# Kernel tuning notes

Hardware: AMD Instinct MI355X
Metric: run time of the kernel (lower is better)

Reference implementation:

```python
import jax, jax.numpy as jnp
from jax import lax
import numpy as np

B, CIN, CP, H, W = 16, 64, 64, 64, 64
K1 = 3   # deformable kernel
K2 = 5   # parallel conv kernel
EPS = 1e-5


def conv2d(x, w, stride, pad):
    return lax.conv_general_dilated(
        x, w, (stride, stride), [(pad, pad), (pad, pad)],
        dimension_numbers=('NCHW', 'OIHW', 'NCHW'))


def batchnorm(x, g, b, m, v):
    scale = g / jnp.sqrt(v + EPS)
    return (x - m[None, :, None, None]) * scale[None, :, None, None] + b[None, :, None, None]


def deform_conv2d(x, offset, weight, stride, pad):
    # x: [B,Cin,H,W], offset: [B,2*K*K,Ho,Wo] (dy,dx interleaved per kernel tap, torchvision layout)
    Bn, Cin, Hn, Wn = x.shape
    Cout, _, K, _ = weight.shape
    KK = K * K
    Ho, Wo = offset.shape[2], offset.shape[3]
    off = offset.reshape(Bn, KK, 2, Ho, Wo)
    dy, dx = off[:, :, 0], off[:, :, 1]                      # [B,KK,Ho,Wo]
    ky, kx = jnp.meshgrid(jnp.arange(K), jnp.arange(K), indexing='ij')
    ky = ky.reshape(KK).astype(x.dtype)
    kx = kx.reshape(KK).astype(x.dtype)
    base_y = (jnp.arange(Ho) * stride - pad).astype(x.dtype)
    base_x = (jnp.arange(Wo) * stride - pad).astype(x.dtype)
    ys = base_y[None, None, :, None] + ky[None, :, None, None] + dy  # [B,KK,Ho,Wo]
    xs = base_x[None, None, None, :] + kx[None, :, None, None] + dx
    y0 = jnp.floor(ys); x0 = jnp.floor(xs)
    wy1 = ys - y0; wx1 = xs - x0
    wy0 = 1.0 - wy1; wx0 = 1.0 - wx1
    flat = x.reshape(Bn, Cin, Hn * Wn)

    def gather(yi, xi):
        valid = ((yi >= 0) & (yi <= Hn - 1) & (xi >= 0) & (xi <= Wn - 1))
        yc = jnp.clip(yi, 0, Hn - 1).astype(jnp.int32)
        xc = jnp.clip(xi, 0, Wn - 1).astype(jnp.int32)
        idx = (yc * Wn + xc).reshape(Bn, -1)                 # [B,KK*Ho*Wo]
        g = jax.vmap(lambda f, i: jnp.take(f, i, axis=1))(flat, idx)
        g = g.reshape(Bn, Cin, KK, Ho, Wo)
        return g * valid.astype(x.dtype)[:, None]

    val = (gather(y0, x0) * (wy0 * wx0)[:, None]
           + gather(y0, x0 + 1) * (wy0 * wx1)[:, None]
           + gather(y0 + 1, x0) * (wy1 * wx0)[:, None]
           + gather(y0 + 1, x0 + 1) * (wy1 * wx1)[:, None])   # [B,Cin,KK,Ho,Wo]
    w_r = weight.reshape(Cout, Cin, KK)
    return jnp.einsum('bcknm,ock->bonm', val, w_r)


def setup_inputs():
    key = jax.random.key(0)
    ks = jax.random.split(key, 18)
    f32 = jnp.float32
    x = jax.random.normal(ks[0], (B, CIN, H, W), f32)
    w_off = jax.random.normal(ks[1], (2 * K1 * K1, CIN, 3, 3), f32) * 0.01
    b_off = jnp.zeros((2 * K1 * K1,), f32)
    w1 = jax.random.normal(ks[2], (CP, CIN, K1, K1), f32) / np.sqrt(CIN * K1 * K1)
    w3 = jax.random.normal(ks[3], (CP, CIN, K2, K2), f32) / np.sqrt(CIN * K2 * K2)
    w2 = jax.random.normal(ks[4], (CP, CP, 3, 3), f32) / np.sqrt(CP * 9)
    def bn(i):
        g = jax.random.uniform(ks[5 + 4 * i], (CP,), f32, 0.5, 1.5)
        b = jax.random.normal(ks[6 + 4 * i], (CP,), f32) * 0.1
        m = jax.random.normal(ks[7 + 4 * i], (CP,), f32) * 0.1
        v = jax.random.uniform(ks[8 + 4 * i], (CP,), f32, 0.5, 1.5)
        return g, b, m, v
    g1, b1, m1, v1 = bn(0)
    g3, b3, m3, v3 = bn(1)
    g2, b2, m2, v2 = bn(2)
    return dict(x=x, w_off=w_off, b_off=b_off, w1=w1, g1=g1, b1=b1, m1=m1, v1=v1,
                w3=w3, g3=g3, b3=b3, m3=m3, v3=v3, w2=w2, g2=g2, b2=b2, m2=m2, v2=v2)


def reference(x, w_off, b_off, w1, g1, b1, m1, v1, w3, g3, b3, m3, v3, w2, g2, b2, m2, v2):
    offset1 = conv2d(x, w_off, 1, 1) + b_off[None, :, None, None]
    out = jax.nn.relu(batchnorm(deform_conv2d(x, offset1, w1, 1, 1), g1, b1, m1, v1))
    out_1 = jax.nn.relu(batchnorm(conv2d(x, w3, 1, 2), g3, b3, m3, v3))
    out = out + out_1
    out = batchnorm(conv2d(out, w2, 1, 1), g2, b2, m2, v2)
    out = out + x  # identity shortcut (stride=1, in_planes==planes)
    return jax.nn.relu(out)
```

## Files before the change

kernel.cpp:

```cpp
#include <hip/hip_runtime.h>
#include <hip/hip_bf16.h>


#define HWv 4096
#define EPSv 1e-5f

typedef __attribute__((ext_vector_type(8))) short bf16x8;
typedef __attribute__((ext_vector_type(16))) float f32x16;
typedef __attribute__((ext_vector_type(2))) float f32x2;

__device__ inline ushort f2bf(float f) {
  __hip_bfloat16 h = __float2bfloat16(f);
  return *(ushort*)&h;
}
__device__ inline float bf2f(ushort u) {
  unsigned int t = ((unsigned int)u) << 16;
  union { unsigned int i; float f; } c; c.i = t; return c.f;
}
__device__ inline float bitsf(unsigned int u) {
  union { unsigned int i; float f; } c; c.i = u; return c.f;
}

__global__ __launch_bounds__(256) void prep_kernel(
    const float* __restrict__ x, const float* __restrict__ w3,
    const float* __restrict__ w2, const float* __restrict__ w1,
    const float* __restrict__ w_off,
    ushort* __restrict__ xT, ushort* __restrict__ w3F,
    ushort* __restrict__ w2F, ushort* __restrict__ w1F,
    ushort* __restrict__ wofF) {
  __shared__ float tile[64][65];
  const int blk = blockIdx.x;
  if (blk < 1024) {
    const int y = blk & 63, b = blk >> 6;
    for (int i = threadIdx.x; i < 4096; i += 256) {
      int ci = i >> 6, xx = i & 63;
      tile[ci][xx] = x[(((size_t)b * 64 + ci) * 64 + y) * 64 + xx];
    }
    __syncthreads();
    for (int i = threadIdx.x; i < 2048; i += 256) {
      int xx = i >> 5, cip = (i & 31) * 2;
      ushort2 v;
      v.x = f2bf(tile[cip][xx]);
      v.y = f2bf(tile[cip + 1][xx]);
      *(ushort2*)&xT[(((size_t)b * 64 + y) * 64 + xx) * 64 + cip] = v;
    }
    return;
  }
  int idx = (blk - 1024) * 256 + threadIdx.x;
  if (idx < 102400) {
    int j = idx & 7, lane = (idx >> 3) & 63, ks = (idx >> 9) & 3;
    int half = (idx >> 11) & 1, kk = idx >> 12;
    int ln = lane & 31, kh = lane >> 5;
    int co = half * 32 + ln, ci = ks * 16 + kh * 8 + j;
    w3F[idx] = f2bf(w3[(co * 64 + ci) * 25 + kk]);
    return;
  }
  idx -= 102400;
  if (idx < 36864) {
    int j = idx & 7, lane = (idx >> 3) & 63, ks = (idx >> 9) & 3;
    int half = (idx >> 11) & 1, kk = idx >> 12;
    int ln = lane & 31, kh = lane >> 5;
    int co = half * 32 + ln, ci = ks * 16 + kh * 8 + j;
    w2F[idx] = f2bf(w2[(co * 64 + ci) * 9 + kk]);
    return;
  }
  idx -= 36864;
  if (idx < 36864) {
    int j = idx & 7, lane = (idx >> 3) & 63, ks = (idx >> 9) & 3;
    int half = (idx >> 11) & 1, kk = idx >> 12;
    int ln = lane & 31, kh = lane >> 5;
    int co = half * 32 + ln, ci = ks * 16 + kh * 8 + j;
    w1F[idx] = f2bf(w1[(co * 64 + ci) * 9 + kk]);
    return;
  }
  idx -= 36864;
  if (idx < 18432) {
    int j = idx & 7, lane = (idx >> 3) & 63, ks = (idx >> 9) & 3;
    int kk = idx >> 11;
    int ln = lane & 31, kh = lane >> 5;
    int ci = ks * 16 + kh * 8 + j;
    wofF[idx] = f2bf(ln < 18 ? w_off[(ln * 64 + ci) * 9 + kk] : 0.f);
  }
}

__device__ __forceinline__ bf16x8 blend4(bf16x8 va, bf16x8 vb, bf16x8 vc, bf16x8 vd,
                                         f32x2 w00v, f32x2 w01v, f32x2 w10v, f32x2 w11v) {
  const unsigned int* ua = (const unsigned int*)&va;
  const unsigned int* ub = (const unsigned int*)&vb;
  const unsigned int* uc = (const unsigned int*)&vc;
  const unsigned int* ud = (const unsigned int*)&vd;
  bf16x8 f;
  ushort2* fo = (ushort2*)&f;
#pragma unroll
  for (int d = 0; d < 4; ++d) {
    f32x2 av = {bitsf(ua[d] << 16), bitsf(ua[d] & 0xFFFF0000u)};
    f32x2 bv = {bitsf(ub[d] << 16), bitsf(ub[d] & 0xFFFF0000u)};
    f32x2 cv = {bitsf(uc[d] << 16), bitsf(uc[d] & 0xFFFF0000u)};
    f32x2 dv = {bitsf(ud[d] << 16), bitsf(ud[d] & 0xFFFF0000u)};
    f32x2 r = w00v * av + w01v * bv + w10v * cv + w11v * dv;
    __hip_bfloat162 h2 = __float22bfloat162_rn(make_float2(r.x, r.y));
    fo[d] = *(ushort2*)&h2;
  }
  return f;
}

__global__ __launch_bounds__(256, 2) void fused_kernel(
    const ushort* __restrict__ xT, const ushort* __restrict__ wofF,
    const float* __restrict__ b_off, const ushort* __restrict__ w1F,
    const ushort* __restrict__ w3F,
    const float* __restrict__ g1, const float* __restrict__ b1,
    const float* __restrict__ m1, const float* __restrict__ v1,
    const float* __restrict__ g3, const float* __restrict__ b3,
    const float* __restrict__ m3, const float* __restrict__ v3,
    ushort* __restrict__ s1T) {
  __shared__ __align__(16) uint4 ldsx[6 * 68 * 8];
  __shared__ float stash[2 * 64 * 18];
  __shared__ float bn1s[64], bn1b[64], bn3s[64], bn3b[64];

  const int tid = threadIdx.x;
  const int wv = tid >> 6, lane = tid & 63;
  const int ln = lane & 31, kh = lane >> 5;
  const int r = wv >> 1, nt = wv & 1;
  const int y0 = blockIdx.x * 2, b = blockIdx.y;
  const int y = y0 + r, px = nt * 32 + ln;
  const uint4* xT4 = (const uint4*)xT;
  const bool interior = (y0 >= 2 && y0 <= 60);

  if (tid < 64) {
    float s = g1[tid] * rsqrtf(v1[tid] + EPSv);
    bn1s[tid] = s; bn1b[tid] = b1[tid] - m1[tid] * s;
    float s3 = g3[tid] * rsqrtf(v3[tid] + EPSv);
    bn3s[tid] = s3; bn3b[tid] = b3[tid] - m3[tid] * s3;
  }
  for (int i = tid; i < 6 * 68 * 8; i += 256) {
    int tr = i / (68 * 8), rem = i % (68 * 8);
    int col = rem >> 3, c = rem & 7;
    int ysrc = min(max(y0 - 2 + tr, 0), 63);
    int xcol = col - 2;
    uint4 v = make_uint4(0, 0, 0, 0);
    if (xcol >= 0 && xcol <= 63)
      v = xT4[((size_t)((b * 64 + ysrc) * 64 + xcol)) * 8 + c];
    ldsx[(tr * 68 + col) * 8 + (c ^ (col & 7))] = v;
  }
  __syncthreads();

  f32x16 acco;
#pragma unroll
  for (int j = 0; j < 16; ++j) acco[j] = 0.f;
  if (interior) {
#pragma unroll
    for (int kk = 0; kk < 9; ++kk) {
      const int ky = kk / 3, kx = kk % 3;
      const int tr = r + ky + 1;
      const int col = px + kx + 1;
      bf16x8 af[4], bf[4];
#pragma unroll
      for (int ks = 0; ks < 4; ++ks)
        af[ks] = *(const bf16x8*)&wofF[(size_t)((kk * 4 + ks) * 64 + lane) * 8];
#pragma unroll
      for (int ks = 0; ks < 4; ++ks) {
        int c = ks * 2 + kh;
        bf[ks] = *(const bf16x8*)&ldsx[(tr * 68 + col) * 8 + (c ^ (col & 7))];
      }
#pragma unroll
      for (int ks = 0; ks < 4; ++ks)
        acco = __builtin_amdgcn_mfma_f32_32x32x16_bf16(af[ks], bf[ks], acco, 0, 0, 0);
    }
  } else {
#pragma unroll
    for (int kk = 0; kk < 9; ++kk) {
      const int ky = kk / 3, kx = kk % 3;
      const int yy = y - 1 + ky;
      if (yy >= 0 && yy <= 63) {
        const int tr = yy - (y0 - 2);
        const int col = px + kx + 1;
#pragma unroll
        for (int ks = 0; ks < 4; ++ks) {
          int c = ks * 2 + kh;
          bf16x8 af = *(const bf16x8*)&wofF[(size_t)((kk * 4 + ks) * 64 + lane) * 8];
          bf16x8 bf = *(const bf16x8*)&ldsx[(tr * 68 + col) * 8 + (c ^ (col & 7))];
          acco = __builtin_amdgcn_mfma_f32_32x32x16_bf16(af, bf, acco, 0, 0, 0);
        }
      }
    }
  }
#pragma unroll
  for (int reg = 0; reg < 16; ++reg) {
    int co = (reg & 3) + 8 * (reg >> 2) + 4 * kh;
    if (co < 18)
      stash[(r * 64 + px) * 18 + co] = acco[reg] + b_off[co];
  }
  __syncthreads();

  float dyv[9], dxv[9];
#pragma unroll
  for (int kk = 0; kk < 9; ++kk) {
    dyv[kk] = stash[(r * 64 + px) * 18 + 2 * kk];
    dxv[kk] = stash[(r * 64 + px) * 18 + 2 * kk + 1];
  }
  bool fast = true;
#pragma unroll
  for (int kk = 0; kk < 9; ++kk) {
    int iy0 = (int)floorf((float)(y - 1 + kk / 3) + dyv[kk]);
    int iy1 = iy0 + 1;
    bool ok0 = (iy0 < 0) || (iy0 > 63) || (iy0 >= y0 - 2 && iy0 <= y0 + 3);
    bool ok1 = (iy1 < 0) || (iy1 > 63) || (iy1 >= y0 - 2 && iy1 <= y0 + 3);
    fast = fast && ok0 && ok1;
  }

  f32x16 accd0, accd1;
#pragma unroll
  for (int j = 0; j < 16; ++j) { accd0[j] = 0.f; accd1[j] = 0.f; }
  const ushort* xb = xT + (size_t)b * 64 * 64 * 64;

  if (__ballot(!fast) == 0ull) {
#pragma unroll
    for (int kk = 0; kk < 9; ++kk) {
      const int ky = kk / 3, kx = kk % 3;
      float ys = (float)(y - 1 + ky) + dyv[kk];
      float xs = (float)(px - 1 + kx) + dxv[kk];
      float y0f = floorf(ys), x0f = floorf(xs);
      float wy1 = ys - y0f, wx1 = xs - x0f;
      float wy0 = 1.f - wy1, wx0 = 1.f - wx1;
      int iy0 = (int)y0f, ix0 = (int)x0f;
      int iy1 = iy0 + 1, ix1 = ix0 + 1;
      float vy0 = (iy0 >= 0 && iy0 <= 63) ? 1.f : 0.f;
      float vy1 = (iy1 >= 0 && iy1 <= 63) ? 1.f : 0.f;
      float vx0 = (ix0 >= 0 && ix0 <= 63) ? 1.f : 0.f;
      float vx1 = (ix1 >= 0 && ix1 <= 63) ? 1.f : 0.f;
      int x0c = min(max(ix0, 0), 63), x1c = min(max(ix1, 0), 63);
      float w00 = wy0 * wx0 * vy0 * vx0;
      float w01 = wy0 * wx1 * vy0 * vx1;
      float w10 = wy1 * wx0 * vy1 * vx0;
      float w11 = wy1 * wx1 * vy1 * vx1;
      int tr0 = min(max(iy0 - (y0 - 2), 0), 5);
      int tr1 = min(max(iy1 - (y0 - 2), 0), 5);
      int c0 = x0c + 2, c1 = x1c + 2;
      f32x2 w00v = {w00, w00}, w01v = {w01, w01};
      f32x2 w10v = {w10, w10}, w11v = {w11, w11};

      bf16x8 a0[4], a1[4], va[4], vb[4], vc[4], vd[4];
#pragma unroll
      for (int ks = 0; ks < 4; ++ks) {
        a0[ks] = *(const bf16x8*)&w1F[(size_t)(((kk * 2 + 0) * 4 + ks) * 64 + lane) * 8];
        a1[ks] = *(const bf16x8*)&w1F[(size_t)(((kk * 2 + 1) * 4 + ks) * 64 + lane) * 8];
      }
#pragma unroll
      for (int ks = 0; ks < 4; ++ks) {
        int c = ks * 2 + kh;
        va[ks] = *(const bf16x8*)&ldsx[(tr0 * 68 + c0) * 8 + (c ^ (c0 & 7))];
        vb[ks] = *(const bf16x8*)&ldsx[(tr0 * 68 + c1) * 8 + (c ^ (c1 & 7))];
        vc[ks] = *(const bf16x8*)&ldsx[(tr1 * 68 + c0) * 8 + (c ^ (c0 & 7))];
        vd[ks] = *(const bf16x8*)&ldsx[(tr1 * 68 + c1) * 8 + (c ^ (c1 & 7))];
      }
#pragma unroll
      for (int ks = 0; ks < 4; ++ks) {
        bf16x8 f = blend4(va[ks], vb[ks], vc[ks], vd[ks], w00v, w01v, w10v, w11v);
        accd0 = __builtin_amdgcn_mfma_f32_32x32x16_bf16(a0[ks], f, accd0, 0, 0, 0);
        accd1 = __builtin_amdgcn_mfma_f32_32x32x16_bf16(a1[ks], f, accd1, 0, 0, 0);
      }
    }
  } else {
#pragma unroll
    for (int kk = 0; kk < 9; ++kk) {
      const int ky = kk / 3, kx = kk % 3;
      float ys = (float)(y - 1 + ky) + dyv[kk];
      float xs = (float)(px - 1 + kx) + dxv[kk];
      float y0f = floorf(ys), x0f = floorf(xs);
      float wy1 = ys - y0f, wx1 = xs - x0f;
      float wy0 = 1.f - wy1, wx0 = 1.f - wx1;
      int iy0 = (int)y0f, ix0 = (int)x0f;
      int iy1 = iy0 + 1, ix1 = ix0 + 1;
      float vy0 = (iy0 >= 0 && iy0 <= 63) ? 1.f : 0.f;
      float vy1 = (iy1 >= 0 && iy1 <= 63) ? 1.f : 0.f;
      float vx0 = (ix0 >= 0 && ix0 <= 63) ? 1.f : 0.f;
      float vx1 = (ix1 >= 0 && ix1 <= 63) ? 1.f : 0.f;
      int x0c = min(max(ix0, 0), 63), x1c = min(max(ix1, 0), 63);
      float w00 = wy0 * wx0 * vy0 * vx0;
      float w01 = wy0 * wx1 * vy0 * vx1;
      float w10 = wy1 * wx0 * vy1 * vx0;
      float w11 = wy1 * wx1 * vy1 * vx1;
      int tr0 = min(max(iy0 - (y0 - 2), 0), 5);
      int tr1 = min(max(iy1 - (y0 - 2), 0), 5);
      int c0 = x0c + 2, c1 = x1c + 2;
      f32x2 w00v = {w00, w00}, w01v = {w01, w01};
      f32x2 w10v = {w10, w10}, w11v = {w11, w11};

      bf16x8 frag[4];
#pragma unroll
      for (int ks = 0; ks < 4; ++ks) {
        int c = ks * 2 + kh;
        bf16x8 va = *(const bf16x8*)&ldsx[(tr0 * 68 + c0) * 8 + (c ^ (c0 & 7))];
        bf16x8 vb = *(const bf16x8*)&ldsx[(tr0 * 68 + c1) * 8 + (c ^ (c1 & 7))];
        bf16x8 vc = *(const bf16x8*)&ldsx[(tr1 * 68 + c0) * 8 + (c ^ (c0 & 7))];
        bf16x8 vd = *(const bf16x8*)&ldsx[(tr1 * 68 + c1) * 8 + (c ^ (c1 & 7))];
        frag[ks] = blend4(va, vb, vc, vd, w00v, w01v, w10v, w11v);
      }
      if (!fast) {
        int y0c = min(max(iy0, 0), 63), y1c = min(max(iy1, 0), 63);
        const ushort* p00 = xb + (y0c * 64 + x0c) * 64 + kh * 8;
        const ushort* p01 = xb + (y0c * 64 + x1c) * 64 + kh * 8;
        const ushort* p10 = xb + (y1c * 64 + x0c) * 64 + kh * 8;
        const ushort* p11 = xb + (y1c * 64 + x1c) * 64 + kh * 8;
#pragma unroll
        for (int ks = 0; ks < 4; ++ks) {
          bf16x8 va = *(const bf16x8*)(p00 + ks * 16);
          bf16x8 vb = *(const bf16x8*)(p01 + ks * 16);
          bf16x8 vc = *(const bf16x8*)(p10 + ks * 16);
          bf16x8 vd = *(const bf16x8*)(p11 + ks * 16);
          frag[ks] = blend4(va, vb, vc, vd, w00v, w01v, w10v, w11v);
        }
      }
#pragma unroll
      for (int ks = 0; ks < 4; ++ks) {
        bf16x8 a0 = *(const bf16x8*)&w1F[(size_t)(((kk * 2 + 0) * 4 + ks) * 64 + lane) * 8];
        bf16x8 a1 = *(const bf16x8*)&w1F[(size_t)(((kk * 2 + 1) * 4 + ks) * 64 + lane) * 8];
        accd0 = __builtin_amdgcn_mfma_f32_32x32x16_bf16(a0, frag[ks], accd0, 0, 0, 0);
        accd1 = __builtin_amdgcn_mfma_f32_32x32x16_bf16(a1, frag[ks], accd1, 0, 0, 0);
      }
    }
  }

  f32x16 acc50, acc51;
#pragma unroll
  for (int j = 0; j < 16; ++j) { acc50[j] = 0.f; acc51[j] = 0.f; }
  if (interior) {
#pragma unroll
    for (int kk = 0; kk < 25; ++kk) {
      const int ky = kk / 5, kx = kk % 5;
      const int tr = r + ky;
      const int col = px + kx;
      bf16x8 a0[4], a1[4], bfv[4];
#pragma unroll
      for (int ks = 0; ks < 4; ++ks) {
        a0[ks] = *(const bf16x8*)&w3F[(size_t)(((kk * 2 + 0) * 4 + ks) * 64 + lane) * 8];
        a1[ks] = *(const bf16x8*)&w3F[(size_t)(((kk * 2 + 1) * 4 + ks) * 64 + lane) * 8];
      }
#pragma unroll
      for (int ks = 0; ks < 4; ++ks) {
        int c = ks * 2 + kh;
        bfv[ks] = *(const bf16x8*)&ldsx[(tr * 68 + col) * 8 + (c ^ (col & 7))];
      }
#pragma unroll
      for (int ks = 0; ks < 4; ++ks) {
        acc50 = __builtin_amdgcn_mfma_f32_32x32x16_bf16(a0[ks], bfv[ks], acc50, 0, 0, 0);
        acc51 = __builtin_amdgcn_mfma_f32_32x32x16_bf16(a1[ks], bfv[ks], acc51, 0, 0, 0);
      }
    }
  } else {
#pragma unroll
    for (int kk = 0; kk < 25; ++kk) {
      const int ky = kk / 5, kx = kk % 5;
      const int yy = y - 2 + ky;
      if (yy >= 0 && yy <= 63) {
        const int tr = r + ky;
        const int col = px + kx;
#pragma unroll
        for (int ks = 0; ks < 4; ++ks) {
          int c = ks * 2 + kh;
          bf16x8 bf = *(const bf16x8*)&ldsx[(tr * 68 + col) * 8 + (c ^ (col & 7))];
          bf16x8 a0 = *(const bf16x8*)&w3F[(size_t)(((kk * 2 + 0) * 4 + ks) * 64 + lane) * 8];
          bf16x8 a1 = *(const bf16x8*)&w3F[(size_t)(((kk * 2 + 1) * 4 + ks) * 64 + lane) * 8];
          acc50 = __builtin_amdgcn_mfma_f32_32x32x16_bf16(a0, bf, acc50, 0, 0, 0);
          acc51 = __builtin_amdgcn_mfma_f32_32x32x16_bf16(a1, bf, acc51, 0, 0, 0);
        }
      }
    }
  }

  ushort* op = s1T + ((size_t)((b * 64 + y) * 64 + px)) * 64;
#pragma unroll
  for (int q = 0; q < 4; ++q) {
    int co0 = 8 * q + 4 * kh;
    float vv[4];
#pragma unroll
    for (int rr = 0; rr < 4; ++rr) {
      int co = co0 + rr;
      float vd = accd0[q * 4 + rr] * bn1s[co] + bn1b[co];
      vd = vd > 0.f ? vd : 0.f;
      float v5 = acc50[q * 4 + rr] * bn3s[co] + bn3b[co];
      v5 = v5 > 0.f ? v5 : 0.f;
      vv[rr] = vd + v5;
    }
    ushort4 st;
    st.x = f2bf(vv[0]); st.y = f2bf(vv[1]); st.z = f2bf(vv[2]); st.w = f2bf(vv[3]);
    *(ushort4*)(op + co0) = st;
#pragma unroll
    for (int rr = 0; rr < 4; ++rr) {
      int co = co0 + 32 + rr;
      float vd = accd1[q * 4 + rr] * bn1s[co] + bn1b[co];
      vd = vd > 0.f ? vd : 0.f;
      float v5 = acc51[q * 4 + rr] * bn3s[co] + bn3b[co];
      v5 = v5 > 0.f ? v5 : 0.f;
      vv[rr] = vd + v5;
    }
    st.x = f2bf(vv[0]); st.y = f2bf(vv[1]); st.z = f2bf(vv[2]); st.w = f2bf(vv[3]);
    *(ushort4*)(op + co0 + 32) = st;
  }
}

__global__ __launch_bounds__(256, 2) void conv3_mfma_kernel(
    const ushort* __restrict__ s1T, const ushort* __restrict__ w2F,
    const float* __restrict__ g2, const float* __restrict__ b2,
    const float* __restrict__ m2, const float* __restrict__ v2,
    const float* __restrict__ x, float* __restrict__ out) {
  __shared__ __align__(16) uint4 Bt[3 * 66 * 8];
  __shared__ float sc[64], bi[64];
  const int tid = threadIdx.x;
  if (tid < 64) {
    float s = g2[tid] * rsqrtf(v2[tid] + EPSv);
    sc[tid] = s;
    bi[tid] = b2[tid] - m2[tid] * s;
  }
  const int y = blockIdx.x, b = blockIdx.y;
  const int wv = tid >> 6, lane = tid & 63;
  const int ln = lane & 31, kh = lane >> 5;
  const int mh = wv & 1, nt = wv >> 1;
  const int px = nt * 32 + ln;
  const uint4* s1T4 = (const uint4*)s1T;

  for (int i = tid; i < 3 * 66 * 8; i += 256) {
    int tr = i / (66 * 8), rem = i % (66 * 8);
    int col = rem >> 3, c = rem & 7;
    int yy = y - 1 + tr, xcol = col - 1;
    uint4 v = make_uint4(0, 0, 0, 0);
    if (yy >= 0 && yy <= 63 && xcol >= 0 && xcol <= 63)
      v = s1T4[((size_t)((b * 64 + yy) * 64 + xcol)) * 8 + c];
    Bt[(tr * 66 + col) * 8 + (c ^ (col & 7))] = v;
  }
  __syncthreads();

  f32x16 acc;
#pragma unroll
  for (int j = 0; j < 16; ++j) acc[j] = 0.f;

#pragma unroll
  for (int kk = 0; kk < 9; ++kk) {
    const int ky = kk / 3, kx = kk % 3;
    const int col = px + kx;
    bf16x8 af[4], bfr[4];
#pragma unroll
    for (int ccb = 0; ccb < 4; ++ccb)
      af[ccb] = *(const bf16x8*)&w2F[(size_t)(((kk * 2 + mh) * 4 + ccb) * 64 + lane) * 8];
#pragma unroll
    for (int ccb = 0; ccb < 4; ++ccb) {
      int c = ccb * 2 + kh;
      bfr[ccb] = *(const bf16x8*)&Bt[(ky * 66 + col) * 8 + (c ^ (col & 7))];
    }
#pragma unroll
    for (int ccb = 0; ccb < 4; ++ccb)
      acc = __builtin_amdgcn_mfma_f32_32x32x16_bf16(af[ccb], bfr[ccb], acc, 0, 0, 0);
  }
#pragma unroll
  for (int reg = 0; reg < 16; ++reg) {
    int co = (reg & 3) + 8 * (reg >> 2) + 4 * kh + mh * 32;
    size_t o = (((size_t)b * 64 + co) * 64 + y) * 64 + px;
    float v = acc[reg] * sc[co] + bi[co] + x[o];
    out[o] = v > 0.f ? v : 0.f;
  }
}

extern "C" void kernel_launch(void* const* d_in, const int* in_sizes, int n_in,
                              void* d_out, int out_size, void* d_ws, size_t ws_size,
                              hipStream_t stream) {
  const float* x     = (const float*)d_in[0];
  const float* w_off = (const float*)d_in[1];
  const float* b_off = (const float*)d_in[2];
  const float* w1    = (const float*)d_in[3];
  const float* g1    = (const float*)d_in[4];
  const float* b1    = (const float*)d_in[5];
  const float* m1    = (const float*)d_in[6];
  const float* v1    = (const float*)d_in[7];
  const float* w3    = (const float*)d_in[8];
  const float* g3    = (const float*)d_in[9];
  const float* b3    = (const float*)d_in[10];
  const float* m3    = (const float*)d_in[11];
  const float* v3    = (const float*)d_in[12];
  const float* w2    = (const float*)d_in[13];
  const float* g2    = (const float*)d_in[14];
  const float* b2    = (const float*)d_in[15];
  const float* m2    = (const float*)d_in[16];
  const float* v2    = (const float*)d_in[17];
  float* out = (float*)d_out;

  ushort* xT   = (ushort*)d_ws;
  ushort* s1T  = xT + (size_t)16 * 64 * HWv;
  ushort* w3F  = s1T + (size_t)16 * 64 * HWv;
  ushort* w2F  = w3F + 102400;
  ushort* w1F  = w2F + 36864;
  ushort* wofF = w1F + 36864;

  prep_kernel<<<dim3(1024 + 760), dim3(256), 0, stream>>>(x, w3, w2, w1, w_off,
                                                          xT, w3F, w2F, w1F, wofF);
  fused_kernel<<<dim3(32, 16), dim3(256), 0, stream>>>(xT, wofF, b_off, w1F, w3F,
                                                       g1, b1, m1, v1, g3, b3, m3, v3,
                                                       s1T);
  conv3_mfma_kernel<<<dim3(64, 16), dim3(256), 0, stream>>>(s1T, w2F, g2, b2, m2, v2,
                                                            x, out);
}
```

Baseline: 69.00 us.

## Split fused kernel into deform and 5x5 conv wave roles with 512 threads

Doubles the fused kernel's block to 512 threads and gives each wave a role. Role-0 waves do the deformable-conv sampling and MFMA, role-1 waves do the 5x5 parallel conv, and the offset-conv K-dimension is split across both roles with partial sums added through LDS. The 5x5 accumulators are passed to the role-0 waves through swizzled shared memory for the fused BN/ReLU epilogue. This aims to run the two heavy branches concurrently on more waves, since the grid of 512 blocks otherwise underfills the GPU. The cost is more shared memory (about 70KB), extra barriers and an LDS round trip, and the two roles do unequal amounts of work (9 versus 25 taps).

```diff
diff --git a/kernel.cpp b/kernel.cpp
--- a/kernel.cpp
+++ b/kernel.cpp
@@ -12,10 +12,6 @@
 __device__ inline ushort f2bf(float f) {
   __hip_bfloat16 h = __float2bfloat16(f);
   return *(ushort*)&h;
-}
-__device__ inline float bf2f(ushort u) {
-  unsigned int t = ((unsigned int)u) << 16;
-  union { unsigned int i; float f; } c; c.i = t; return c.f;
 }
 __device__ inline float bitsf(unsigned int u) {
   union { unsigned int i; float f; } c; c.i = u; return c.f;
@@ -104,7 +100,7 @@
   return f;
 }
 
-__global__ __launch_bounds__(256, 2) void fused_kernel(
+__global__ __launch_bounds__(512, 4) void fused_kernel(
     const ushort* __restrict__ xT, const ushort* __restrict__ wofF,
     const float* __restrict__ b_off, const ushort* __restrict__ w1F,
     const ushort* __restrict__ w3F,
@@ -113,14 +109,18 @@
     const float* __restrict__ g3, const float* __restrict__ b3,
     const float* __restrict__ m3, const float* __restrict__ v3,
     ushort* __restrict__ s1T) {
-  __shared__ __align__(16) uint4 ldsx[6 * 68 * 8];
-  __shared__ float stash[2 * 64 * 18];
-  __shared__ float bn1s[64], bn1b[64], bn3s[64], bn3b[64];
+  __shared__ __align__(16) unsigned char smem[71680];
+  uint4* ldsx = (uint4*)smem;
+  float* stash = (float*)(smem + 52224);
+  float* bn1s = (float*)(smem + 70656);
+  float* bn1b = bn1s + 64;
+  float* bn3s = bn1s + 128;
+  float* bn3b = bn1s + 192;
 
   const int tid = threadIdx.x;
   const int wv = tid >> 6, lane = tid & 63;
   const int ln = lane & 31, kh = lane >> 5;
-  const int r = wv >> 1, nt = wv & 1;
+  const int role = wv & 1, nt = (wv >> 1) & 1, r = wv >> 2;
   const int y0 = blockIdx.x * 2, b = blockIdx.y;
   const int y = y0 + r, px = nt * 32 + ln;
   const uint4* xT4 = (const uint4*)xT;
@@ -132,7 +132,7 @@
     float s3 = g3[tid] * rsqrtf(v3[tid] + EPSv);
     bn3s[tid] = s3; bn3b[tid] = b3[tid] - m3[tid] * s3;
   }
-  for (int i = tid; i < 6 * 68 * 8; i += 256) {
+  for (int i = tid; i < 6 * 68 * 8; i += 512) {
     int tr = i / (68 * 8), rem = i % (68 * 8);
     int col = rem >> 3, c = rem & 7;
     int ysrc = min(max(y0 - 2 + tr, 0), 63);
@@ -144,159 +144,141 @@
   }
   __syncthreads();
 
-  f32x16 acco;
-#pragma unroll
-  for (int j = 0; j < 16; ++j) acco[j] = 0.f;
-  if (interior) {
-#pragma unroll
-    for (int kk = 0; kk < 9; ++kk) {
-      const int ky = kk / 3, kx = kk % 3;
-      const int tr = r + ky + 1;
-      const int col = px + kx + 1;
-      bf16x8 af[4], bf[4];
-#pragma unroll
-      for (int ks = 0; ks < 4; ++ks)
-        af[ks] = *(const bf16x8*)&wofF[(size_t)((kk * 4 + ks) * 64 + lane) * 8];
-#pragma unroll
-      for (int ks = 0; ks < 4; ++ks) {
-        int c = ks * 2 + kh;
-        bf[ks] = *(const bf16x8*)&ldsx[(tr * 68 + col) * 8 + (c ^ (col & 7))];
-      }
-#pragma unroll
-      for (int ks = 0; ks < 4; ++ks)
-        acco = __builtin_amdgcn_mfma_f32_32x32x16_bf16(af[ks], bf[ks], acco, 0, 0, 0);
-    }
-  } else {
-#pragma unroll
-    for (int kk = 0; kk < 9; ++kk) {
-      const int ky = kk / 3, kx = kk % 3;
-      const int yy = y - 1 + ky;
-      if (yy >= 0 && yy <= 63) {
-        const int tr = yy - (y0 - 2);
+  {
+    f32x16 acco;
+#pragma unroll
+    for (int j = 0; j < 16; ++j) acco[j] = 0.f;
+    if (interior) {
+#pragma unroll
+      for (int kk = 0; kk < 9; ++kk) {
+        const int ky = kk / 3, kx = kk % 3;
+        const int tr = r + ky + 1;
         const int col = px + kx + 1;
 #pragma unroll
-        for (int ks = 0; ks < 4; ++ks) {
+        for (int ksq = 0; ksq < 2; ++ksq) {
+          int ks = role * 2 + ksq;
           int c = ks * 2 + kh;
           bf16x8 af = *(const bf16x8*)&wofF[(size_t)((kk * 4 + ks) * 64 + lane) * 8];
           bf16x8 bf = *(const bf16x8*)&ldsx[(tr * 68 + col) * 8 + (c ^ (col & 7))];
           acco = __builtin_amdgcn_mfma_f32_32x32x16_bf16(af, bf, acco, 0, 0, 0);
         }
       }
-    }
-  }
-#pragma unroll
-  for (int reg = 0; reg < 16; ++reg) {
-    int co = (reg & 3) + 8 * (reg >> 2) + 4 * kh;
-    if (co < 18)
-      stash[(r * 64 + px) * 18 + co] = acco[reg] + b_off[co];
+    } else {
+#pragma unroll
+      for (int kk = 0; kk < 9; ++kk) {
+        const int ky = kk / 3, kx = kk % 3;
+        const int yy = y - 1 + ky;
+        if (yy >= 0 && yy <= 63) {
+          const int tr = yy - (y0 - 2);
+          const int col = px + kx + 1;
+#pragma unroll
+          for (int ksq = 0; ksq < 2; ++ksq) {
+            int ks = role * 2 + ksq;
+            int c = ks * 2 + kh;
+            bf16x8 af = *(const bf16x8*)&wofF[(size_t)((kk * 4 + ks) * 64 + lane) * 8];
+            bf16x8 bf = *(const bf16x8*)&ldsx[(tr * 68 + col) * 8 + (c ^ (col & 7))];
+            acco = __builtin_amdgcn_mfma_f32_32x32x16_bf16(af, bf, acco, 0, 0, 0);
+          }
+        }
+      }
+    }
+    float* stb = stash + role * 2304;
+#pragma unroll
+    for (int reg = 0; reg < 16; ++reg) {
+      int co = (reg & 3) + 8 * (reg >> 2) + 4 * kh;
+      if (co < 18)
+        stb[(r * 64 + px) * 18 + co] = acco[reg] + (role ? 0.f : b_off[co]);
+    }
   }
   __syncthreads();
 
-  float dyv[9], dxv[9];
-#pragma unroll
-  for (int kk = 0; kk < 9; ++kk) {
-    dyv[kk] = stash[(r * 64 + px) * 18 + 2 * kk];
-    dxv[kk] = stash[(r * 64 + px) * 18 + 2 * kk + 1];
-  }
-  bool fast = true;
-#pragma unroll
-  for (int kk = 0; kk < 9; ++kk) {
-    int iy0 = (int)floorf((float)(y - 1 + kk / 3) + dyv[kk]);
-    int iy1 = iy0 + 1;
-    bool ok0 = (iy0 < 0) || (iy0 > 63) || (iy0 >= y0 - 2 && iy0 <= y0 + 3);
-    bool ok1 = (iy1 < 0) || (iy1 > 63) || (iy1 >= y0 - 2 && iy1 <= y0 + 3);
-    fast = fast && ok0 && ok1;
-  }
-
-  f32x16 accd0, accd1;
-#pragma unroll
-  for (int j = 0; j < 16; ++j) { accd0[j] = 0.f; accd1[j] = 0.f; }
-  const ushort* xb = xT + (size_t)b * 64 * 64 * 64;
-
-  if (__ballot(!fast) == 0ull) {
+  f32x16 accA, accB;
+#pragma unroll
+  for (int j = 0; j < 16; ++j) { accA[j] = 0.f; accB[j] = 0.f; }
+
+  if (role == 0) {
+    float dyv[9], dxv[9];
+    const int sb = (r * 64 + px) * 18;
 #pragma unroll
     for (int kk = 0; kk < 9; ++kk) {
-      const int ky = kk / 3, kx = kk % 3;
-      float ys = (float)(y - 1 + ky) + dyv[kk];
-      float xs = (float)(px - 1 + kx) + dxv[kk];
-      float y0f = floorf(ys), x0f = floorf(xs);
-      float wy1 = ys - y0f, wx1 = xs - x0f;
-      float wy0 = 1.f - wy1, wx0 = 1.f - wx1;
-      int iy0 = (int)y0f, ix0 = (int)x0f;
-      int iy1 = iy0 + 1, ix1 = ix0 + 1;
-      float vy0 = (iy0 >= 0 && iy0 <= 63) ? 1.f : 0.f;
-      float vy1 = (iy1 >= 0 && iy1 <= 63) ? 1.f : 0.f;
-      float vx0 = (ix0 >= 0 && ix0 <= 63) ? 1.f : 0.f;
-      float vx1 = (ix1 >= 0 && ix1 <= 63) ? 1.f : 0.f;
-      int x0c = min(max(ix0, 0), 63), x1c = min(max(ix1, 0), 63);
-      float w00 = wy0 * wx0 * vy0 * vx0;
-      float w01 = wy0 * wx1 * vy0 * vx1;
-      float w10 = wy1 * wx0 * vy1 * vx0;
-      float w11 = wy1 * wx1 * vy1 * vx1;
-      int tr0 = min(max(iy0 - (y0 - 2), 0), 5);
-      int tr1 = min(max(iy1 - (y0 - 2), 0), 5);
-      int c0 = x0c + 2, c1 = x1c + 2;
-      f32x2 w00v = {w00, w00}, w01v = {w01, w01};
-      f32x2 w10v = {w10, w10}, w11v = {w11, w11};
-
-      bf16x8 a0[4], a1[4], va[4], vb[4], vc[4], vd[4];
-#pragma unroll
-      for (int ks = 0; ks < 4; ++ks) {
-        a0[ks] = *(const bf16x8*)&w1F[(size_t)(((kk * 2 + 0) * 4 + ks) * 64 + lane) * 8];
-        a1[ks] = *(const bf16x8*)&w1F[(size_t)(((kk * 2 + 1) * 4 + ks) * 64 + lane) * 8];
-      }
-#pragma unroll
-      for (int ks = 0; ks < 4; ++ks) {
-        int c = ks * 2 + kh;
-        va[ks] = *(const bf16x8*)&ldsx[(tr0 * 68 + c0) * 8 + (c ^ (c0 & 7))];
-        vb[ks] = *(const bf16x8*)&ldsx[(tr0 * 68 + c1) * 8 + (c ^ (c1 & 7))];
-        vc[ks] = *(const bf16x8*)&ldsx[(tr1 * 68 + c0) * 8 + (c ^ (c0 & 7))];
-        vd[ks] = *(const bf16x8*)&ldsx[(tr1 * 68 + c1) * 8 + (c ^ (c1 & 7))];
-      }
-#pragma unroll
-      for (int ks = 0; ks < 4; ++ks) {
-        bf16x8 f = blend4(va[ks], vb[ks], vc[ks], vd[ks], w00v, w01v, w10v, w11v);
-        accd0 = __builtin_amdgcn_mfma_f32_32x32x16_bf16(a0[ks], f, accd0, 0, 0, 0);
-        accd1 = __builtin_amdgcn_mfma_f32_32x32x16_bf16(a1[ks], f, accd1, 0, 0, 0);
-      }
-    }
-  } else {
+      dyv[kk] = stash[sb + 2 * kk] + stash[2304 + sb + 2 * kk];
+      dxv[kk] = stash[sb + 2 * kk + 1] + stash[2304 + sb + 2 * kk + 1];
+    }
+    bool fast = true;
 #pragma unroll
     for (int kk = 0; kk < 9; ++kk) {
-      const int ky = kk / 3, kx = kk % 3;
-      float ys = (float)(y - 1 + ky) + dyv[kk];
-      float xs = (float)(px - 1 + kx) + dxv[kk];
-      float y0f = floorf(ys), x0f = floorf(xs);
-      float wy1 = ys - y0f, wx1 = xs - x0f;
-      float wy0 = 1.f - wy1, wx0 = 1.f - wx1;
-      int iy0 = (int)y0f, ix0 = (int)x0f;
-      int iy1 = iy0 + 1, ix1 = ix0 + 1;
-      float vy0 = (iy0 >= 0 && iy0 <= 63) ? 1.f : 0.f;
-      float vy1 = (iy1 >= 0 && iy1 <= 63) ? 1.f : 0.f;
-      float vx0 = (ix0 >= 0 && ix0 <= 63) ? 1.f : 0.f;
-      float vx1 = (ix1 >= 0 && ix1 <= 63) ? 1.f : 0.f;
-      int x0c = min(max(ix0, 0), 63), x1c = min(max(ix1, 0), 63);
-      float w00 = wy0 * wx0 * vy0 * vx0;
-      float w01 = wy0 * wx1 * vy0 * vx1;
-      float w10 = wy1 * wx0 * vy1 * vx0;
-      float w11 = wy1 * wx1 * vy1 * vx1;
-      int tr0 = min(max(iy0 - (y0 - 2), 0), 5);
-      int tr1 = min(max(iy1 - (y0 - 2), 0), 5);
-      int c0 = x0c + 2, c1 = x1c + 2;
-      f32x2 w00v = {w00, w00}, w01v = {w01, w01};
-      f32x2 w10v = {w10, w10}, w11v = {w11, w11};
-
-      bf16x8 frag[4];
-#pragma unroll
-      for (int ks = 0; ks < 4; ++ks) {
-        int c = ks * 2 + kh;
-        bf16x8 va = *(const bf16x8*)&ldsx[(tr0 * 68 + c0) * 8 + (c ^ (c0 & 7))];
-        bf16x8 vb = *(const bf16x8*)&ldsx[(tr0 * 68 + c1) * 8 + (c ^ (c1 & 7))];
-        bf16x8 vc = *(const bf16x8*)&ldsx[(tr1 * 68 + c0) * 8 + (c ^ (c0 & 7))];
-        bf16x8 vd = *(const bf16x8*)&ldsx[(tr1 * 68 + c1) * 8 + (c ^ (c1 & 7))];
-        frag[ks] = blend4(va, vb, vc, vd, w00v, w01v, w10v, w11v);
-      }
-      if (!fast) {
+      int iy0 = (int)floorf((float)(y - 1 + kk / 3) + dyv[kk]);
+      int iy1 = iy0 + 1;
+      bool ok0 = (iy0 < 0) || (iy0 > 63) || (iy0 >= y0 - 2 && iy0 <= y0 + 3);
+      bool ok1 = (iy1 < 0) || (iy1 > 63) || (iy1 >= y0 - 2 && iy1 <= y0 + 3);
+      fast = fast && ok0 && ok1;
+    }
+    const ushort* xb = xT + (size_t)b * 64 * 64 * 64;
+
+    if (__ballot(!fast) == 0ull) {
+#pragma unroll
+      for (int kk = 0; kk < 9; ++kk) {
+        const int ky = kk / 3, kx = kk % 3;
+        float ys = (float)(y - 1 + ky) + dyv[kk];
+        float xs = (float)(px - 1 + kx) + dxv[kk];
+        float y0f = floorf(ys), x0f = floorf(xs);
+        float wy1 = ys - y0f, wx1 = xs - x0f;
+        float wy0 = 1.f - wy1, wx0 = 1.f - wx1;
+        int iy0 = (int)y0f, ix0 = (int)x0f;
+        int iy1 = iy0 + 1, ix1 = ix0 + 1;
+        float vy0 = (iy0 >= 0 && iy0 <= 63) ? 1.f : 0.f;
+        float vy1 = (iy1 >= 0 && iy1 <= 63) ? 1.f : 0.f;
+        float vx0 = (ix0 >= 0 && ix0 <= 63) ? 1.f : 0.f;
+        float vx1 = (ix1 >= 0 && ix1 <= 63) ? 1.f : 0.f;
+        int x0c = min(max(ix0, 0), 63), x1c = min(max(ix1, 0), 63);
+        float w00 = wy0 * wx0 * vy0 * vx0;
+        float w01 = wy0 * wx1 * vy0 * vx1;
+        float w10 = wy1 * wx0 * vy1 * vx0;
+        float w11 = wy1 * wx1 * vy1 * vx1;
+        int tr0 = min(max(iy0 - (y0 - 2), 0), 5);
+        int tr1 = min(max(iy1 - (y0 - 2), 0), 5);
+        int c0 = x0c + 2, c1 = x1c + 2;
+        f32x2 w00v = {w00, w00}, w01v = {w01, w01};
+        f32x2 w10v = {w10, w10}, w11v = {w11, w11};
+#pragma unroll
+        for (int ks = 0; ks < 4; ++ks) {
+          int c = ks * 2 + kh;
+          bf16x8 va = *(const bf16x8*)&ldsx[(tr0 * 68 + c0) * 8 + (c ^ (c0 & 7))];
+          bf16x8 vb = *(const bf16x8*)&ldsx[(tr0 * 68 + c1) * 8 + (c ^ (c1 & 7))];
+          bf16x8 vc = *(const bf16x8*)&ldsx[(tr1 * 68 + c0) * 8 + (c ^ (c0 & 7))];
+          bf16x8 vd = *(const bf16x8*)&ldsx[(tr1 * 68 + c1) * 8 + (c ^ (c1 & 7))];
+          bf16x8 f = blend4(va, vb, vc, vd, w00v, w01v, w10v, w11v);
+          bf16x8 a0 = *(const bf16x8*)&w1F[(size_t)(((kk * 2 + 0) * 4 + ks) * 64 + lane) * 8];
+          bf16x8 a1 = *(const bf16x8*)&w1F[(size_t)(((kk * 2 + 1) * 4 + ks) * 64 + lane) * 8];
+          accA = __builtin_amdgcn_mfma_f32_32x32x16_bf16(a0, f, accA, 0, 0, 0);
+          accB = __builtin_amdgcn_mfma_f32_32x32x16_bf16(a1, f, accB, 0, 0, 0);
+        }
+      }
+    } else {
+#pragma unroll
+      for (int kk = 0; kk < 9; ++kk) {
+        const int ky = kk / 3, kx = kk % 3;
+        float ys = (float)(y - 1 + ky) + dyv[kk];
+        float xs = (float)(px - 1 + kx) + dxv[kk];
+        float y0f = floorf(ys), x0f = floorf(xs);
+        float wy1 = ys - y0f, wx1 = xs - x0f;
+        float wy0 = 1.f - wy1, wx0 = 1.f - wx1;
+        int iy0 = (int)y0f, ix0 = (int)x0f;
+        int iy1 = iy0 + 1, ix1 = ix0 + 1;
+        float vy0 = (iy0 >= 0 && iy0 <= 63) ? 1.f : 0.f;
+        float vy1 = (iy1 >= 0 && iy1 <= 63) ? 1.f : 0.f;
+        float vx0 = (ix0 >= 0 && ix0 <= 63) ? 1.f : 0.f;
+        float vx1 = (ix1 >= 0 && ix1 <= 63) ? 1.f : 0.f;
+        int x0c = min(max(ix0, 0), 63), x1c = min(max(ix1, 0), 63);
+        float w00 = wy0 * wx0 * vy0 * vx0;
+        float w01 = wy0 * wx1 * vy0 * vx1;
+        float w10 = wy1 * wx0 * vy1 * vx0;
+        float w11 = wy1 * wx1 * vy1 * vx1;
+        int tr0 = min(max(iy0 - (y0 - 2), 0), 5);
+        int tr1 = min(max(iy1 - (y0 - 2), 0), 5);
+        int c0 = x0c + 2, c1 = x1c + 2;
+        f32x2 w00v = {w00, w00}, w01v = {w01, w01};
+        f32x2 w10v = {w10, w10}, w11v = {w11, w11};
         int y0c = min(max(iy0, 0), 63), y1c = min(max(iy1, 0), 63);
         const ushort* p00 = xb + (y0c * 64 + x0c) * 64 + kh * 8;
         const ushort* p01 = xb + (y0c * 64 + x1c) * 64 + kh * 8;
@@ -304,98 +286,120 @@
         const ushort* p11 = xb + (y1c * 64 + x1c) * 64 + kh * 8;
 #pragma unroll
         for (int ks = 0; ks < 4; ++ks) {
-          bf16x8 va = *(const bf16x8*)(p00 + ks * 16);
-          bf16x8 vb = *(const bf16x8*)(p01 + ks * 16);
-          bf16x8 vc = *(const bf16x8*)(p10 + ks * 16);
-          bf16x8 vd = *(const bf16x8*)(p11 + ks * 16);
-          frag[ks] = blend4(va, vb, vc, vd, w00v, w01v, w10v, w11v);
-        }
-      }
-#pragma unroll
-      for (int ks = 0; ks < 4; ++ks) {
-        bf16x8 a0 = *(const bf16x8*)&w1F[(size_t)(((kk * 2 + 0) * 4 + ks) * 64 + lane) * 8];
-        bf16x8 a1 = *(const bf16x8*)&w1F[(size_t)(((kk * 2 + 1) * 4 + ks) * 64 + lane) * 8];
-        accd0 = __builtin_amdgcn_mfma_f32_32x32x16_bf16(a0, frag[ks], accd0, 0, 0, 0);
-        accd1 = __builtin_amdgcn_mfma_f32_32x32x16_bf16(a1, frag[ks], accd1, 0, 0, 0);
-      }
-    }
-  }
-
-  f32x16 acc50, acc51;
-#pragma unroll
-  for (int j = 0; j < 16; ++j) { acc50[j] = 0.f; acc51[j] = 0.f; }
-  if (interior) {
-#pragma unroll
-    for (int kk = 0; kk < 25; ++kk) {
-      const int ky = kk / 5, kx = kk % 5;
-      const int tr = r + ky;
-      const int col = px + kx;
-      bf16x8 a0[4], a1[4], bfv[4];
-#pragma unroll
-      for (int ks = 0; ks < 4; ++ks) {
-        a0[ks] = *(const bf16x8*)&w3F[(size_t)(((kk * 2 + 0) * 4 + ks) * 64 + lane) * 8];
-        a1[ks] = *(const bf16x8*)&w3F[(size_t)(((kk * 2 + 1) * 4 + ks) * 64 + lane) * 8];
-      }
-#pragma unroll
-      for (int ks = 0; ks < 4; ++ks) {
-        int c = ks * 2 + kh;
-        bfv[ks] = *(const bf16x8*)&ldsx[(tr * 68 + col) * 8 + (c ^ (col & 7))];
-      }
-#pragma unroll
-      for (int ks = 0; ks < 4; ++ks) {
-        acc50 = __builtin_amdgcn_mfma_f32_32x32x16_bf16(a0[ks], bfv[ks], acc50, 0, 0, 0);
-        acc51 = __builtin_amdgcn_mfma_f32_32x32x16_bf16(a1[ks], bfv[ks], acc51, 0, 0, 0);
+          int c = ks * 2 + kh;
+          bf16x8 va = *(const bf16x8*)&ldsx[(tr0 * 68 + c0) * 8 + (c ^ (c0 & 7))];
+          bf16x8 vb = *(const bf16x8*)&ldsx[(tr0 * 68 + c1) * 8 + (c ^ (c1 & 7))];
+          bf16x8 vc = *(const bf16x8*)&ldsx[(tr1 * 68 + c0) * 8 + (c ^ (c0 & 7))];
+          bf16x8 vd = *(const bf16x8*)&ldsx[(tr1 * 68 + c1) * 8 + (c ^ (c1 & 7))];
+          bf16x8 f = blend4(va, vb, vc, vd, w00v, w01v, w10v, w11v);
+          if (!fast) {
+            bf16x8 ga = *(const bf16x8*)(p00 + ks * 16);
+            bf16x8 gb = *(const bf16x8*)(p01 + ks * 16);
+            bf16x8 gc = *(const bf16x8*)(p10 + ks * 16);
+            bf16x8 gd = *(const bf16x8*)(p11 + ks * 16);
+            f = blend4(ga, gb, gc, gd, w00v, w01v, w10v, w11v);
+          }
+          bf16x8 a0 = *(const bf16x8*)&w1F[(size_t)(((kk * 2 + 0) * 4 + ks) * 64 + lane) * 8];
+          bf16x8 a1 = *(const bf16x8*)&w1F[(size_t)(((kk * 2 + 1) * 4 + ks) * 64 + lane) * 8];
+          accA = __builtin_amdgcn_mfma_f32_32x32x16_bf16(a0, f, accA, 0, 0, 0);
+          accB = __builtin_amdgcn_mfma_f32_32x32x16_bf16(a1, f, accB, 0, 0, 0);
+        }
       }
     }
   } else {
-#pragma unroll
-    for (int kk = 0; kk < 25; ++kk) {
-      const int ky = kk / 5, kx = kk % 5;
-      const int yy = y - 2 + ky;
-      if (yy >= 0 && yy <= 63) {
+    if (interior) {
+#pragma unroll
+      for (int kk = 0; kk < 25; ++kk) {
+        const int ky = kk / 5, kx = kk % 5;
         const int tr = r + ky;
         const int col = px + kx;
+        bf16x8 a0[4], a1[4], bfv[4];
+#pragma unroll
+        for (int ks = 0; ks < 4; ++ks) {
+          a0[ks] = *(const bf16x8*)&w3F[(size_t)(((kk * 2 + 0) * 4 + ks) * 64 + lane) * 8];
+          a1[ks] = *(const bf16x8*)&w3F[(size_t)(((kk * 2 + 1) * 4 + ks) * 64 + lane) * 8];
+        }
 #pragma unroll
         for (int ks = 0; ks < 4; ++ks) {
           int c = ks * 2 + kh;
-          bf16x8 bf = *(const bf16x8*)&ldsx[(tr * 68 + col) * 8 + (c ^ (col & 7))];
-          bf16x8 a0 = *(const bf16x8*)&w3F[(size_t)(((kk * 2 + 0) * 4 + ks) * 64 + lane) * 8];
-          bf16x8 a1 = *(const bf16x8*)&w3F[(size_t)(((kk * 2 + 1) * 4 + ks) * 64 + lane) * 8];
-          acc50 = __builtin_amdgcn_mfma_f32_32x32x16_bf16(a0, bf, acc50, 0, 0, 0);
-          acc51 = __builtin_amdgcn_mfma_f32_32x32x16_bf16(a1, bf, acc51, 0, 0, 0);
-        }
-      }
-    }
-  }
-
-  ushort* op = s1T + ((size_t)((b * 64 + y) * 64 + px)) * 64;
-#pragma unroll
-  for (int q = 0; q < 4; ++q) {
-    int co0 = 8 * q + 4 * kh;
-    float vv[4];
-#pragma unroll
-    for (int rr = 0; rr < 4; ++rr) {
-      int co = co0 + rr;
-      float vd = accd0[q * 4 + rr] * bn1s[co] + bn1b[co];
-      vd = vd > 0.f ? vd : 0.f;
-      float v5 = acc50[q * 4 + rr] * bn3s[co] + bn3b[co];
-      v5 = v5 > 0.f ? v5 : 0.f;
-      vv[rr] = vd + v5;
-    }
-    ushort4 st;
-    st.x = f2bf(vv[0]); st.y = f2bf(vv[1]); st.z = f2bf(vv[2]); st.w = f2bf(vv[3]);
-    *(ushort4*)(op + co0) = st;
-#pragma unroll
-    for (int rr = 0; rr < 4; ++rr) {
-      int co = co0 + 32 + rr;
-      float vd = accd1[q * 4 + rr] * bn1s[co] + bn1b[co];
-      vd = vd > 0.f ? vd : 0.f;
-      float v5 = acc51[q * 4 + rr] * bn3s[co] + bn3b[co];
-      v5 = v5 > 0.f ? v5 : 0.f;
-      vv[rr] = vd + v5;
-    }
-    st.x = f2bf(vv[0]); st.y = f2bf(vv[1]); st.z = f2bf(vv[2]); st.w = f2bf(vv[3]);
-    *(ushort4*)(op + co0 + 32) = st;
+          bfv[ks] = *(const bf16x8*)&ldsx[(tr * 68 + col) * 8 + (c ^ (col & 7))];
+        }
+#pragma unroll
+        for (int ks = 0; ks < 4; ++ks) {
+          accA = __builtin_amdgcn_mfma_f32_32x32x16_bf16(a0[ks], bfv[ks], accA, 0, 0, 0);
+          accB = __builtin_amdgcn_mfma_f32_32x32x16_bf16(a1[ks], bfv[ks], accB, 0, 0, 0);
+        }
+      }
+    } else {
+#pragma unroll
+      for (int kk = 0; kk < 25; ++kk) {
+        const int ky = kk / 5, kx = kk % 5;
+        const int yy = y - 2 + ky;
+        if (yy >= 0 && yy <= 63) {
+          const int tr = r + ky;
+          const int col = px + kx;
+#pragma unroll
+          for (int ks = 0; ks < 4; ++ks) {
+            int c = ks * 2 + kh;
+            bf16x8 bf = *(const bf16x8*)&ldsx[(tr * 68 + col) * 8 + (c ^ (col & 7))];
+            bf16x8 a0 = *(const bf16x8*)&w3F[(size_t)(((kk * 2 + 0) * 4 + ks) * 64 + lane) * 8];
+            bf16x8 a1 = *(const bf16x8*)&w3F[(size_t)(((kk * 2 + 1) * 4 + ks) * 64 + lane) * 8];
+            accA = __builtin_amdgcn_mfma_f32_32x32x16_bf16(a0, bf, accA, 0, 0, 0);
+            accB = __builtin_amdgcn_mfma_f32_32x32x16_bf16(a1, bf, accB, 0, 0, 0);
+          }
+        }
+      }
+    }
+  }
+
+  __syncthreads();
+  float4* sp = (float4*)((float*)smem + ((size_t)((r * 2 + nt) * 64 + lane)) * 32);
+  const int sw = lane & 7;
+  if (role) {
+    union { f32x16 v; float4 q[4]; } ua, ub;
+    ua.v = accA; ub.v = accB;
+    sp[0 ^ sw] = ua.q[0]; sp[1 ^ sw] = ua.q[1];
+    sp[2 ^ sw] = ua.q[2]; sp[3 ^ sw] = ua.q[3];
+    sp[4 ^ sw] = ub.q[0]; sp[5 ^ sw] = ub.q[1];
+    sp[6 ^ sw] = ub.q[2]; sp[7 ^ sw] = ub.q[3];
+  }
+  __syncthreads();
+  if (!role) {
+    union { f32x16 v; float4 q[4]; } ua, ub;
+    ua.q[0] = sp[0 ^ sw]; ua.q[1] = sp[1 ^ sw];
+    ua.q[2] = sp[2 ^ sw]; ua.q[3] = sp[3 ^ sw];
+    ub.q[0] = sp[4 ^ sw]; ub.q[1] = sp[5 ^ sw];
+    ub.q[2] = sp[6 ^ sw]; ub.q[3] = sp[7 ^ sw];
+
+    ushort* op = s1T + ((size_t)((b * 64 + y) * 64 + px)) * 64;
+#pragma unroll
+    for (int q = 0; q < 4; ++q) {
+      int co0 = 8 * q + 4 * kh;
+      float vv[4];
+#pragma unroll
+      for (int rr = 0; rr < 4; ++rr) {
+        int co = co0 + rr;
+        float vd = accA[q * 4 + rr] * bn1s[co] + bn1b[co];
+        vd = vd > 0.f ? vd : 0.f;
+        float v5 = ua.v[q * 4 + rr] * bn3s[co] + bn3b[co];
+        v5 = v5 > 0.f ? v5 : 0.f;
+        vv[rr] = vd + v5;
+      }
+      ushort4 st;
+      st.x = f2bf(vv[0]); st.y = f2bf(vv[1]); st.z = f2bf(vv[2]); st.w = f2bf(vv[3]);
+      *(ushort4*)(op + co0) = st;
+#pragma unroll
+      for (int rr = 0; rr < 4; ++rr) {
+        int co = co0 + 32 + rr;
+        float vd = accB[q * 4 + rr] * bn1s[co] + bn1b[co];
+        vd = vd > 0.f ? vd : 0.f;
+        float v5 = ub.v[q * 4 + rr] * bn3s[co] + bn3b[co];
+        v5 = v5 > 0.f ? v5 : 0.f;
+        vv[rr] = vd + v5;
+      }
+      st.x = f2bf(vv[0]); st.y = f2bf(vv[1]); st.z = f2bf(vv[2]); st.w = f2bf(vv[3]);
+      *(ushort4*)(op + co0 + 32) = st;
+    }
   }
 }
 
@@ -492,7 +496,7 @@
 
   prep_kernel<<<dim3(1024 + 760), dim3(256), 0, stream>>>(x, w3, w2, w1, w_off,
                                                           xT, w3F, w2F, w1F, wofF);
-  fused_kernel<<<dim3(32, 16), dim3(256), 0, stream>>>(xT, wofF, b_off, w1F, w3F,
+  fused_kernel<<<dim3(32, 16), dim3(512), 0, stream>>>(xT, wofF, b_off, w1F, w3F,
                                                        g1, b1, m1, v1, g3, b3, m3, v3,
                                                        s1T);
   conv3_mfma_kernel<<<dim3(64, 16), dim3(256), 0, stream>>>(s1T, w2F, g2, b2, m2, v2,
```

Result: no change. 70.37 us (+2.0%).
